# Kernel optimization log

Hardware: AMD Instinct MI355X
Metric: run time of the kernel (lower is better)

Reference implementation:

```python
import jax, jax.numpy as jnp
import numpy as np

NUM_EDGE_TYPES = 8
HIDDEN = 128
N_NODES = 50000
N_EDGES = 600000


def setup_inputs() -> dict:
    key = jax.random.key(0)
    ks = jax.random.split(key, 10)
    H = HIDDEN
    h = jax.random.normal(ks[0], (N_NODES, H), dtype=jnp.float32)
    edge_index = jax.random.randint(ks[1], (2, N_EDGES), 0, N_NODES, dtype=jnp.int32)
    edge_type = jax.random.randint(ks[2], (N_EDGES,), 0, NUM_EDGE_TYPES + 1, dtype=jnp.int32)
    s = 1.0 / np.sqrt(H)
    W_msg = jax.random.uniform(ks[3], (H, H), jnp.float32, -s, s)
    b_msg = jax.random.uniform(ks[4], (H,), jnp.float32, -s, s)
    edge_embed = jax.random.normal(ks[5], (NUM_EDGE_TYPES + 1, H), dtype=jnp.float32)
    W_ih = jax.random.uniform(ks[6], (3 * H, H), jnp.float32, -s, s)
    W_hh = jax.random.uniform(ks[7], (3 * H, H), jnp.float32, -s, s)
    b_ih = jax.random.uniform(ks[8], (3 * H,), jnp.float32, -s, s)
    b_hh = jax.random.uniform(ks[9], (3 * H,), jnp.float32, -s, s)
    return {"h": h, "edge_index": edge_index, "edge_type": edge_type,
            "num_nodes": N_NODES, "W_msg": W_msg, "b_msg": b_msg,
            "edge_embed": edge_embed, "W_ih": W_ih, "W_hh": W_hh,
            "b_ih": b_ih, "b_hh": b_hh}


def _gru_cell(x, h, W_ih, W_hh, b_ih, b_hh):
    # PyTorch GRUCell: gates ordered (r, z, n)
    H = h.shape[-1]
    gi = x @ W_ih.T + b_ih  # (N, 3H)
    gh = h @ W_hh.T + b_hh
    i_r, i_z, i_n = gi[:, :H], gi[:, H:2 * H], gi[:, 2 * H:]
    h_r, h_z, h_n = gh[:, :H], gh[:, H:2 * H], gh[:, 2 * H:]
    r = jax.nn.sigmoid(i_r + h_r)
    z = jax.nn.sigmoid(i_z + h_z)
    n = jnp.tanh(i_n + r * h_n)
    return (1.0 - z) * n + z * h


def reference(h, edge_index, edge_type, num_nodes, W_msg, b_msg, edge_embed, W_ih, W_hh, b_ih, b_hh):
    src = edge_index[0]
    dst = edge_index[1]
    # gather -> linear -> edge-type embed add
    src_h = h[src] @ W_msg.T + b_msg                      # (E, H)
    emb = edge_embed[jnp.clip(edge_type, 0, NUM_EDGE_TYPES)]  # (E, H)
    msg = src_h + emb
    # scatter-add into per-node message buffer
    messages = jax.ops.segment_sum(msg, dst, num_segments=num_nodes)  # (num_nodes, H)
    h_new = _gru_cell(messages, h[:num_nodes], W_ih, W_hh, b_ih, b_hh)
    result = jnp.zeros_like(h).at[:num_nodes].set(h_new)
    return result
```

## Files before the change

kernel.cpp:

```cpp
#include <hip/hip_runtime.h>
#include <math.h>

#define H 128
typedef unsigned int u32;
typedef unsigned long long u64;
typedef __attribute__((ext_vector_type(8))) short short8;
typedef __attribute__((ext_vector_type(4))) float floatx4;

#define XS_STRIDE 136

#define SCAN_B 64
#define SCAN_T 256

__device__ __forceinline__ float sigmoid_f(float x) {
    return 1.0f / (1.0f + __expf(-x));
}
__device__ __forceinline__ float tanh_f(float x) {
    float t = __expf(-2.0f * fabsf(x));
    float r = (1.0f - t) / (1.0f + t);
    return copysignf(r, x);
}
__device__ __forceinline__ unsigned short f2bf(float x) {
    u32 u = __float_as_uint(x);
    return (unsigned short)((u + 0x7fffu + ((u >> 16) & 1u)) >> 16);
}
__device__ __forceinline__ float bf2f(unsigned short s) {
    return __uint_as_float(((u32)s) << 16);
}
__device__ __forceinline__ float bf_lo32(u32 u) { return __uint_as_float(u << 16); }
__device__ __forceinline__ float bf_hi32(u32 u) { return __uint_as_float(u & 0xffff0000u); }

__global__ __launch_bounds__(256) void h_convert_kernel(
    const float* __restrict__ h, unsigned short* __restrict__ h_b, int total8)
{
    int idx = blockIdx.x * 256 + threadIdx.x;
    if (idx >= total8) return;
    const float4* p = (const float4*)(h + (size_t)idx * 8);
    float4 a = p[0], b = p[1];
    short8 v;
    v[0] = (short)f2bf(a.x); v[1] = (short)f2bf(a.y);
    v[2] = (short)f2bf(a.z); v[3] = (short)f2bf(a.w);
    v[4] = (short)f2bf(b.x); v[5] = (short)f2bf(b.y);
    v[6] = (short)f2bf(b.z); v[7] = (short)f2bf(b.w);
    *(short8*)(h_b + (size_t)idx * 8) = v;
}

__global__ __launch_bounds__(256) void prep_kernel(
    const float* __restrict__ Wih, const float* __restrict__ Whh,
    const float* __restrict__ Wm,  const float* __restrict__ emb,
    const float* __restrict__ bm,
    unsigned short* __restrict__ Wcs, unsigned short* __restrict__ Whhs,
    unsigned short* __restrict__ embWs)
{
    int idx = blockIdx.x * 256 + threadIdx.x;
    if (idx < 49152) {
        int g = idx >> 7;
        int k = idx & 127;
        float acc = 0.f;
#pragma unroll 4
        for (int c = 0; c < H; ++c)
            acc += Wih[(size_t)g * H + c] * Wm[(size_t)c * H + k];
        int gate = g >> 7;
        int wi = g & 127;
        int j = wi >> 4, m = wi & 15;
        int kc = k >> 5, q = (k >> 3) & 3, i = k & 7;
        int l = q * 16 + m;
        Wcs[(size_t)(((gate * 8 + j) * 4 + kc) * 64 + l) * 8 + i] = f2bf(acc);
    } else if (idx < 61440) {
        int s = idx - 49152;
        int i = s & 7;
        int l = (s >> 3) & 63;
        int jb = s >> 9;
        int gate = jb >> 3, jj = jb & 7;
        int q = l >> 4, m = l & 15;
        int t = q * 8 + i;
        unsigned short v = 0;
        if (t < 9) {
            int g = gate * 128 + jj * 16 + m;
            float acc = 0.f;
#pragma unroll 4
            for (int jx = 0; jx < H; ++jx)
                acc += (emb[(size_t)t * H + jx] + bm[jx]) * Wih[(size_t)g * H + jx];
            v = f2bf(acc);
        }
        embWs[s] = v;
    } else if (idx < 67584) {
        int t2 = idx - 61440;
        int l  = t2 & 63;
        int kc = (t2 >> 6) & 3;
        int jr = t2 >> 8;
        int m = l & 15, q = l >> 4;
        size_t srco = (size_t)(jr * 16 + m) * H + kc * 32 + q * 8;
        const float4* s0 = (const float4*)(Whh + srco);
        float4 a = s0[0], b = s0[1];
        short8 v;
        v[0] = (short)f2bf(a.x); v[1] = (short)f2bf(a.y);
        v[2] = (short)f2bf(a.z); v[3] = (short)f2bf(a.w);
        v[4] = (short)f2bf(b.x); v[5] = (short)f2bf(b.y);
        v[6] = (short)f2bf(b.z); v[7] = (short)f2bf(b.w);
        *(short8*)(Whhs + (size_t)t2 * 8) = v;
    }
}

__global__ __launch_bounds__(256) void hist_kernel(
    const int* __restrict__ eidx, int* __restrict__ deg, int E)
{
    int e = blockIdx.x * 256 + threadIdx.x;
    if (e < E) atomicAdd(&deg[eidx[E + e]], 1);
}

__global__ __launch_bounds__(SCAN_T) void scan_part_kernel(
    const int* __restrict__ deg, int* __restrict__ tsum,
    int* __restrict__ bsum, int N, int ipt)
{
    __shared__ int red[SCAN_T];
    int t = threadIdx.x;
    int g = blockIdx.x * SCAN_T + t;
    int s = g * ipt;
    int e = s + ipt < N ? s + ipt : N;
    int sum = 0;
    for (int i = s; i < e; ++i) sum += deg[i];
    tsum[g] = sum;
    red[t] = sum;
    __syncthreads();
    for (int d = SCAN_T / 2; d > 0; d >>= 1) {
        if (t < d) red[t] += red[t + d];
        __syncthreads();
    }
    if (t == 0) bsum[blockIdx.x] = red[0];
}

__global__ __launch_bounds__(SCAN_T) void scan_final_kernel(
    const int* __restrict__ deg, const int* __restrict__ tsum,
    const int* __restrict__ bsum, int* __restrict__ off,
    int* __restrict__ pos, int N, int ipt)
{
    __shared__ int part[SCAN_T];
    __shared__ int bpre[SCAN_B + 1];
    int t = threadIdx.x;
    if (t == 0) {
        int acc = 0;
        for (int b2 = 0; b2 < SCAN_B; ++b2) { bpre[b2] = acc; acc += bsum[b2]; }
        bpre[SCAN_B] = acc;
        if (blockIdx.x == 0) off[N] = acc;
    }
    int g = blockIdx.x * SCAN_T + t;
    part[t] = tsum[g];
    __syncthreads();
    for (int d = 1; d < SCAN_T; d <<= 1) {
        int v = (t >= d) ? part[t - d] : 0;
        __syncthreads();
        part[t] += v;
        __syncthreads();
    }
    int base = bpre[blockIdx.x] + ((t == 0) ? 0 : part[t - 1]);
    int s = g * ipt;
    int e = s + ipt < N ? s + ipt : N;
    for (int i = s; i < e; ++i) {
        off[i] = base;
        pos[i] = base;
        base += deg[i];
    }
}

__global__ __launch_bounds__(256) void fill_kernel(
    const int* __restrict__ eidx, const int* __restrict__ etype,
    int* __restrict__ pos, int* __restrict__ packed, int E)
{
    int e = blockIdx.x * 256 + threadIdx.x;
    if (e >= E) return;
    int src = eidx[e];
    int dst = eidx[E + e];
    int t = etype[e];
    t = t < 0 ? 0 : (t > 8 ? 8 : t);
    int p = atomicAdd(&pos[dst], 1);
    packed[p] = src | (t << 24);
}

__global__ __launch_bounds__(256) void gather_kernel(
    const unsigned short* __restrict__ h_b,
    const int* __restrict__ off, const int* __restrict__ packed,
    unsigned short* __restrict__ S_b, u64* __restrict__ cnt, int N)
{
    int n = blockIdx.x * 4 + (threadIdx.x >> 6);
    if (n >= N) return;
    int lane = threadIdx.x & 63;
    int b = off[n], e = off[n + 1];
    float ax = 0.f, ay = 0.f;
    u64 c = 0;
    int i = b;
    for (; i + 4 <= e; i += 4) {
        int u0 = packed[i + 0];
        int u1 = packed[i + 1];
        int u2 = packed[i + 2];
        int u3 = packed[i + 3];
        u32 x0 = *((const u32*)(h_b + (size_t)(u0 & 0xffffff) * H) + lane);
        u32 x1 = *((const u32*)(h_b + (size_t)(u1 & 0xffffff) * H) + lane);
        u32 x2 = *((const u32*)(h_b + (size_t)(u2 & 0xffffff) * H) + lane);
        u32 x3 = *((const u32*)(h_b + (size_t)(u3 & 0xffffff) * H) + lane);
        c += (1ull << (7 * (u0 >> 24))) + (1ull << (7 * (u1 >> 24)))
           + (1ull << (7 * (u2 >> 24))) + (1ull << (7 * (u3 >> 24)));
        ax += bf_lo32(x0) + bf_lo32(x1) + bf_lo32(x2) + bf_lo32(x3);
        ay += bf_hi32(x0) + bf_hi32(x1) + bf_hi32(x2) + bf_hi32(x3);
    }
    for (; i < e; ++i) {
        int u = packed[i];
        u32 x = *((const u32*)(h_b + (size_t)(u & 0xffffff) * H) + lane);
        c += 1ull << (7 * (u >> 24));
        ax += bf_lo32(x);
        ay += bf_hi32(x);
    }
    u32 o = (u32)f2bf(ax) | ((u32)f2bf(ay) << 16);
    *((u32*)(S_b + (size_t)n * H) + lane) = o;
    if (lane == 0) cnt[n] = c;
}

__global__ __launch_bounds__(256, 4) void gru_mfma_kernel(
    const unsigned short* __restrict__ S_b, const unsigned short* __restrict__ h_b,
    const unsigned short* __restrict__ Wcs, const unsigned short* __restrict__ Whhs,
    const unsigned short* __restrict__ embWs,
    const float* __restrict__ bih, const float* __restrict__ bhh,
    const u64* __restrict__ cnt,
    const int* __restrict__ numn, float* __restrict__ out, int N)
{
    __shared__ unsigned short xs[32 * XS_STRIDE];
    __shared__ unsigned short hsb[32 * XS_STRIDE];
    __shared__ unsigned short cs[32 * 32];

    int tid = threadIdx.x;
    int node0 = blockIdx.x * 32;

    for (int c = tid; c < 512; c += 256) {
        int r = c >> 4;
        int k8 = (c & 15) << 3;
        int n = node0 + r;
        int nc = n < N ? n : N - 1;
        *(short8*)(&xs[r * XS_STRIDE + k8]) =
            *(const short8*)(S_b + (size_t)nc * H + k8);
        *(short8*)(&hsb[r * XS_STRIDE + k8]) =
            *(const short8*)(h_b + (size_t)nc * H + k8);
    }
    for (int c2 = tid; c2 < 1024; c2 += 256) {
        int r = c2 >> 5, t = c2 & 31;
        int n = node0 + r;
        u64 cv = cnt[n < N ? n : N - 1];
        cs[c2] = (t < 9) ? f2bf((float)((u32)(cv >> (7 * t)) & 127u))
                         : (unsigned short)0;
    }
    __syncthreads();

    int lane = tid & 63;
    int wv = tid >> 6;
    int rg = wv & 1;
    int jhalf = wv >> 1;
    int am = lane & 15;
    int aq = lane >> 4;

    short8 ax[4], ahf[4];
    int arow = rg * 16 + am;
#pragma unroll
    for (int kc = 0; kc < 4; ++kc) {
        ax[kc]  = *(const short8*)(&xs[arow * XS_STRIDE + kc * 32 + aq * 8]);
        ahf[kc] = *(const short8*)(&hsb[arow * XS_STRIDE + kc * 32 + aq * 8]);
    }
    short8 acn = *(const short8*)(&cs[arow * 32 + aq * 8]);

    int num_nodes = numn[0];
    floatx4 zero = {0.f, 0.f, 0.f, 0.f};

#pragma unroll
    for (int jt = 0; jt < 4; ++jt) {
        int j = jhalf * 4 + jt;
        floatx4 aIr = zero, aHr = zero, aIz = zero, aHz = zero, aIn = zero, aHn = zero;
        {
            short8 er = *(const short8*)(embWs + (size_t)((0 * 8 + j) * 64 + lane) * 8);
            short8 ez = *(const short8*)(embWs + (size_t)((1 * 8 + j) * 64 + lane) * 8);
            short8 en = *(const short8*)(embWs + (size_t)((2 * 8 + j) * 64 + lane) * 8);
            aIr = __builtin_amdgcn_mfma_f32_16x16x32_bf16(acn, er, aIr, 0, 0, 0);
            aIz = __builtin_amdgcn_mfma_f32_16x16x32_bf16(acn, ez, aIz, 0, 0, 0);
            aIn = __builtin_amdgcn_mfma_f32_16x16x32_bf16(acn, en, aIn, 0, 0, 0);
        }
#pragma unroll
        for (int kc = 0; kc < 4; ++kc) {
            size_t c_r = (size_t)(((0 * 8 + j) * 4 + kc) * 64 + lane) * 8;
            size_t c_z = (size_t)(((1 * 8 + j) * 4 + kc) * 64 + lane) * 8;
            size_t c_n = (size_t)(((2 * 8 + j) * 4 + kc) * 64 + lane) * 8;
            short8 bir = *(const short8*)(Wcs + c_r);
            short8 bhr = *(const short8*)(Whhs + c_r);
            short8 biz = *(const short8*)(Wcs + c_z);
            short8 bhz = *(const short8*)(Whhs + c_z);
            short8 bin = *(const short8*)(Wcs + c_n);
            short8 bhn = *(const short8*)(Whhs + c_n);
            aIr = __builtin_amdgcn_mfma_f32_16x16x32_bf16(ax[kc],  bir, aIr, 0, 0, 0);
            aHr = __builtin_amdgcn_mfma_f32_16x16x32_bf16(ahf[kc], bhr, aHr, 0, 0, 0);
            aIz = __builtin_amdgcn_mfma_f32_16x16x32_bf16(ax[kc],  biz, aIz, 0, 0, 0);
            aHz = __builtin_amdgcn_mfma_f32_16x16x32_bf16(ahf[kc], bhz, aHz, 0, 0, 0);
            aIn = __builtin_amdgcn_mfma_f32_16x16x32_bf16(ax[kc],  bin, aIn, 0, 0, 0);
            aHn = __builtin_amdgcn_mfma_f32_16x16x32_bf16(ahf[kc], bhn, aHn, 0, 0, 0);
        }
        int c = j * 16 + am;
        float b_ir = bih[c],       b_hr = bhh[c];
        float b_iz = bih[128 + c], b_hz = bhh[128 + c];
        float b_in = bih[256 + c], b_hn = bhh[256 + c];
#pragma unroll
        for (int q = 0; q < 4; ++q) {
            int m = aq * 4 + q;
            int node = node0 + rg * 16 + m;
            if (node < N) {
                float r  = sigmoid_f(aIr[q] + b_ir + aHr[q] + b_hr);
                float z  = sigmoid_f(aIz[q] + b_iz + aHz[q] + b_hz);
                float nv = tanh_f((aIn[q] + b_in) + r * (aHn[q] + b_hn));
                float hv = bf2f(hsb[(rg * 16 + m) * XS_STRIDE + c]);
                float o  = (1.0f - z) * nv + z * hv;
                out[(size_t)node * H + c] = (node < num_nodes) ? o : 0.0f;
            }
        }
    }
}

extern "C" void kernel_launch(void* const* d_in, const int* in_sizes, int n_in,
                              void* d_out, int out_size, void* d_ws, size_t ws_size,
                              hipStream_t stream) {
    const float* h    = (const float*)d_in[0];
    const int*  eidx  = (const int*)d_in[1];
    const int*  etype = (const int*)d_in[2];
    const int*  numn  = (const int*)d_in[3];
    const float* Wm   = (const float*)d_in[4];
    const float* bm   = (const float*)d_in[5];
    const float* emb  = (const float*)d_in[6];
    const float* Wih  = (const float*)d_in[7];
    const float* Whh  = (const float*)d_in[8];
    const float* bih  = (const float*)d_in[9];
    const float* bhh  = (const float*)d_in[10];

    int N = in_sizes[0] / H;
    int E = in_sizes[2];

    unsigned short* S_b   = (unsigned short*)d_ws;
    unsigned short* h_b   = S_b + (size_t)N * H;
    unsigned short* Wcs   = h_b + (size_t)N * H;
    unsigned short* Whhs  = Wcs + 3 * H * H;
    unsigned short* embWs = Whhs + 3 * H * H;
    u64* cnt    = (u64*)(embWs + 12288);
    int* deg    = (int*)(cnt + N);
    int* pos    = deg + N;
    int* off    = pos + N;
    int* packed = off + (N + 1);
    int* tsum   = packed + E;
    int* bsum   = tsum + SCAN_B * SCAN_T;

    hipMemsetAsync(deg, 0, (size_t)N * sizeof(int), stream);

    int total8 = N * H / 8;
    h_convert_kernel<<<(total8 + 255) / 256, 256, 0, stream>>>(h, h_b, total8);
    prep_kernel<<<264, 256, 0, stream>>>(Wih, Whh, Wm, emb, bm, Wcs, Whhs, embWs);
    hist_kernel<<<(E + 255) / 256, 256, 0, stream>>>(eidx, deg, E);

    int ipt = (N + SCAN_B * SCAN_T - 1) / (SCAN_B * SCAN_T);
    scan_part_kernel<<<SCAN_B, SCAN_T, 0, stream>>>(deg, tsum, bsum, N, ipt);
    scan_final_kernel<<<SCAN_B, SCAN_T, 0, stream>>>(deg, tsum, bsum, off, pos, N, ipt);

    fill_kernel<<<(E + 255) / 256, 256, 0, stream>>>(eidx, etype, pos, packed, E);

    gather_kernel<<<(N + 3) / 4, 256, 0, stream>>>(h_b, off, packed, S_b, cnt, N);

    int nblk32 = (N + 31) / 32;
    gru_mfma_kernel<<<nblk32, 256, 0, stream>>>(S_b, h_b, Wcs, Whhs, embWs,
                                                bih, bhh, cnt, numn, (float*)d_out, N);
}
```

Before: 237.8 us.

## Fuse preprocessing kernels and retile GRU kernel to 64 nodes per block

Merges the h-to-bf16 conversion, the degree-buffer zeroing (replacing hipMemsetAsync) and the weight prep into one launch, which removes launch and memset overhead. The GRU MFMA kernel now processes 64 nodes per block, with each wave owning two output column tiles across all four row tiles. Each loaded weight fragment is therefore reused across four MFMA row tiles, cutting global weight traffic per node. The cost is more accumulator registers (72 floats per lane for the six gates times four tiles), which may hurt occupancy under launch_bounds(256,4), and A fragments are now re-read from LDS inside the loop.

```diff
diff --git a/kernel.cpp b/kernel.cpp
--- a/kernel.cpp
+++ b/kernel.cpp
@@ -8,6 +8,7 @@
 typedef __attribute__((ext_vector_type(4))) float floatx4;
 
 #define XS_STRIDE 136
+#define CS_STRIDE 40
 
 #define SCAN_B 64
 #define SCAN_T 256
@@ -30,29 +31,35 @@
 __device__ __forceinline__ float bf_lo32(u32 u) { return __uint_as_float(u << 16); }
 __device__ __forceinline__ float bf_hi32(u32 u) { return __uint_as_float(u & 0xffff0000u); }
 
-__global__ __launch_bounds__(256) void h_convert_kernel(
-    const float* __restrict__ h, unsigned short* __restrict__ h_b, int total8)
-{
-    int idx = blockIdx.x * 256 + threadIdx.x;
-    if (idx >= total8) return;
-    const float4* p = (const float4*)(h + (size_t)idx * 8);
-    float4 a = p[0], b = p[1];
-    short8 v;
-    v[0] = (short)f2bf(a.x); v[1] = (short)f2bf(a.y);
-    v[2] = (short)f2bf(a.z); v[3] = (short)f2bf(a.w);
-    v[4] = (short)f2bf(b.x); v[5] = (short)f2bf(b.y);
-    v[6] = (short)f2bf(b.z); v[7] = (short)f2bf(b.w);
-    *(short8*)(h_b + (size_t)idx * 8) = v;
-}
-
-__global__ __launch_bounds__(256) void prep_kernel(
+__global__ __launch_bounds__(256) void fused_pre_kernel(
+    const float* __restrict__ h, unsigned short* __restrict__ h_b, int total8,
+    int* __restrict__ deg, int N,
     const float* __restrict__ Wih, const float* __restrict__ Whh,
     const float* __restrict__ Wm,  const float* __restrict__ emb,
     const float* __restrict__ bm,
     unsigned short* __restrict__ Wcs, unsigned short* __restrict__ Whhs,
-    unsigned short* __restrict__ embWs)
-{
-    int idx = blockIdx.x * 256 + threadIdx.x;
+    unsigned short* __restrict__ embWs, int HB, int DB)
+{
+    int b = blockIdx.x;
+    if (b < HB) {
+        int idx = b * 256 + threadIdx.x;
+        if (idx >= total8) return;
+        const float4* p = (const float4*)(h + (size_t)idx * 8);
+        float4 a = p[0], bb = p[1];
+        short8 v;
+        v[0] = (short)f2bf(a.x);  v[1] = (short)f2bf(a.y);
+        v[2] = (short)f2bf(a.z);  v[3] = (short)f2bf(a.w);
+        v[4] = (short)f2bf(bb.x); v[5] = (short)f2bf(bb.y);
+        v[6] = (short)f2bf(bb.z); v[7] = (short)f2bf(bb.w);
+        *(short8*)(h_b + (size_t)idx * 8) = v;
+        return;
+    }
+    if (b < HB + DB) {
+        int idx = (b - HB) * 256 + threadIdx.x;
+        if (idx < N) deg[idx] = 0;
+        return;
+    }
+    int idx = (b - HB - DB) * 256 + threadIdx.x;
     if (idx < 49152) {
         int g = idx >> 7;
         int k = idx & 127;
@@ -92,12 +99,12 @@
         int m = l & 15, q = l >> 4;
         size_t srco = (size_t)(jr * 16 + m) * H + kc * 32 + q * 8;
         const float4* s0 = (const float4*)(Whh + srco);
-        float4 a = s0[0], b = s0[1];
+        float4 a = s0[0], bb = s0[1];
         short8 v;
-        v[0] = (short)f2bf(a.x); v[1] = (short)f2bf(a.y);
-        v[2] = (short)f2bf(a.z); v[3] = (short)f2bf(a.w);
-        v[4] = (short)f2bf(b.x); v[5] = (short)f2bf(b.y);
-        v[6] = (short)f2bf(b.z); v[7] = (short)f2bf(b.w);
+        v[0] = (short)f2bf(a.x);  v[1] = (short)f2bf(a.y);
+        v[2] = (short)f2bf(a.z);  v[3] = (short)f2bf(a.w);
+        v[4] = (short)f2bf(bb.x); v[5] = (short)f2bf(bb.y);
+        v[6] = (short)f2bf(bb.z); v[7] = (short)f2bf(bb.w);
         *(short8*)(Whhs + (size_t)t2 * 8) = v;
     }
 }
@@ -223,14 +230,14 @@
     const u64* __restrict__ cnt,
     const int* __restrict__ numn, float* __restrict__ out, int N)
 {
-    __shared__ unsigned short xs[32 * XS_STRIDE];
-    __shared__ unsigned short hsb[32 * XS_STRIDE];
-    __shared__ unsigned short cs[32 * 32];
+    __shared__ unsigned short xs[64 * XS_STRIDE];
+    __shared__ unsigned short hsb[64 * XS_STRIDE];
+    __shared__ unsigned short cs[64 * CS_STRIDE];
 
     int tid = threadIdx.x;
-    int node0 = blockIdx.x * 32;
-
-    for (int c = tid; c < 512; c += 256) {
+    int node0 = blockIdx.x * 64;
+
+    for (int c = tid; c < 1024; c += 256) {
         int r = c >> 4;
         int k8 = (c & 15) << 3;
         int n = node0 + r;
@@ -240,45 +247,46 @@
         *(short8*)(&hsb[r * XS_STRIDE + k8]) =
             *(const short8*)(h_b + (size_t)nc * H + k8);
     }
-    for (int c2 = tid; c2 < 1024; c2 += 256) {
-        int r = c2 >> 5, t = c2 & 31;
+    {
+        int r = tid >> 2, tg = tid & 3;
         int n = node0 + r;
         u64 cv = cnt[n < N ? n : N - 1];
-        cs[c2] = (t < 9) ? f2bf((float)((u32)(cv >> (7 * t)) & 127u))
-                         : (unsigned short)0;
+        short8 v = {0, 0, 0, 0, 0, 0, 0, 0};
+        if (tg == 0) {
+#pragma unroll
+            for (int i = 0; i < 8; ++i)
+                v[i] = (short)f2bf((float)((u32)(cv >> (7 * i)) & 127u));
+        } else if (tg == 1) {
+            v[0] = (short)f2bf((float)((u32)(cv >> 56) & 127u));
+        }
+        *(short8*)(&cs[r * CS_STRIDE + tg * 8]) = v;
     }
     __syncthreads();
 
     int lane = tid & 63;
     int wv = tid >> 6;
-    int rg = wv & 1;
-    int jhalf = wv >> 1;
     int am = lane & 15;
     int aq = lane >> 4;
 
-    short8 ax[4], ahf[4];
-    int arow = rg * 16 + am;
-#pragma unroll
-    for (int kc = 0; kc < 4; ++kc) {
-        ax[kc]  = *(const short8*)(&xs[arow * XS_STRIDE + kc * 32 + aq * 8]);
-        ahf[kc] = *(const short8*)(&hsb[arow * XS_STRIDE + kc * 32 + aq * 8]);
-    }
-    short8 acn = *(const short8*)(&cs[arow * 32 + aq * 8]);
-
     int num_nodes = numn[0];
     floatx4 zero = {0.f, 0.f, 0.f, 0.f};
 
 #pragma unroll
-    for (int jt = 0; jt < 4; ++jt) {
-        int j = jhalf * 4 + jt;
-        floatx4 aIr = zero, aHr = zero, aIz = zero, aHz = zero, aIn = zero, aHn = zero;
+    for (int jj = 0; jj < 2; ++jj) {
+        int j = wv * 2 + jj;
+        floatx4 aIr[4], aHr[4], aIz[4], aHz[4], aIn[4], aHn[4];
         {
             short8 er = *(const short8*)(embWs + (size_t)((0 * 8 + j) * 64 + lane) * 8);
             short8 ez = *(const short8*)(embWs + (size_t)((1 * 8 + j) * 64 + lane) * 8);
             short8 en = *(const short8*)(embWs + (size_t)((2 * 8 + j) * 64 + lane) * 8);
-            aIr = __builtin_amdgcn_mfma_f32_16x16x32_bf16(acn, er, aIr, 0, 0, 0);
-            aIz = __builtin_amdgcn_mfma_f32_16x16x32_bf16(acn, ez, aIz, 0, 0, 0);
-            aIn = __builtin_amdgcn_mfma_f32_16x16x32_bf16(acn, en, aIn, 0, 0, 0);
+#pragma unroll
+            for (int rt = 0; rt < 4; ++rt) {
+                short8 acn = *(const short8*)(&cs[(rt * 16 + am) * CS_STRIDE + aq * 8]);
+                aIr[rt] = __builtin_amdgcn_mfma_f32_16x16x32_bf16(acn, er, zero, 0, 0, 0);
+                aIz[rt] = __builtin_amdgcn_mfma_f32_16x16x32_bf16(acn, ez, zero, 0, 0, 0);
+                aIn[rt] = __builtin_amdgcn_mfma_f32_16x16x32_bf16(acn, en, zero, 0, 0, 0);
+                aHr[rt] = zero; aHz[rt] = zero; aHn[rt] = zero;
+            }
         }
 #pragma unroll
         for (int kc = 0; kc < 4; ++kc) {
@@ -291,28 +299,37 @@
             short8 bhz = *(const short8*)(Whhs + c_z);
             short8 bin = *(const short8*)(Wcs + c_n);
             short8 bhn = *(const short8*)(Whhs + c_n);
-            aIr = __builtin_amdgcn_mfma_f32_16x16x32_bf16(ax[kc],  bir, aIr, 0, 0, 0);
-            aHr = __builtin_amdgcn_mfma_f32_16x16x32_bf16(ahf[kc], bhr, aHr, 0, 0, 0);
-            aIz = __builtin_amdgcn_mfma_f32_16x16x32_bf16(ax[kc],  biz, aIz, 0, 0, 0);
-            aHz = __builtin_amdgcn_mfma_f32_16x16x32_bf16(ahf[kc], bhz, aHz, 0, 0, 0);
-            aIn = __builtin_amdgcn_mfma_f32_16x16x32_bf16(ax[kc],  bin, aIn, 0, 0, 0);
-            aHn = __builtin_amdgcn_mfma_f32_16x16x32_bf16(ahf[kc], bhn, aHn, 0, 0, 0);
+#pragma unroll
+            for (int rt = 0; rt < 4; ++rt) {
+                int arow = rt * 16 + am;
+                short8 axv = *(const short8*)(&xs[arow * XS_STRIDE + kc * 32 + aq * 8]);
+                short8 ahv = *(const short8*)(&hsb[arow * XS_STRIDE + kc * 32 + aq * 8]);
+                aIr[rt] = __builtin_amdgcn_mfma_f32_16x16x32_bf16(axv, bir, aIr[rt], 0, 0, 0);
+                aHr[rt] = __builtin_amdgcn_mfma_f32_16x16x32_bf16(ahv, bhr, aHr[rt], 0, 0, 0);
+                aIz[rt] = __builtin_amdgcn_mfma_f32_16x16x32_bf16(axv, biz, aIz[rt], 0, 0, 0);
+                aHz[rt] = __builtin_amdgcn_mfma_f32_16x16x32_bf16(ahv, bhz, aHz[rt], 0, 0, 0);
+                aIn[rt] = __builtin_amdgcn_mfma_f32_16x16x32_bf16(axv, bin, aIn[rt], 0, 0, 0);
+                aHn[rt] = __builtin_amdgcn_mfma_f32_16x16x32_bf16(ahv, bhn, aHn[rt], 0, 0, 0);
+            }
         }
         int c = j * 16 + am;
         float b_ir = bih[c],       b_hr = bhh[c];
         float b_iz = bih[128 + c], b_hz = bhh[128 + c];
         float b_in = bih[256 + c], b_hn = bhh[256 + c];
 #pragma unroll
-        for (int q = 0; q < 4; ++q) {
-            int m = aq * 4 + q;
-            int node = node0 + rg * 16 + m;
-            if (node < N) {
-                float r  = sigmoid_f(aIr[q] + b_ir + aHr[q] + b_hr);
-                float z  = sigmoid_f(aIz[q] + b_iz + aHz[q] + b_hz);
-                float nv = tanh_f((aIn[q] + b_in) + r * (aHn[q] + b_hn));
-                float hv = bf2f(hsb[(rg * 16 + m) * XS_STRIDE + c]);
-                float o  = (1.0f - z) * nv + z * hv;
-                out[(size_t)node * H + c] = (node < num_nodes) ? o : 0.0f;
+        for (int rt = 0; rt < 4; ++rt) {
+#pragma unroll
+            for (int q = 0; q < 4; ++q) {
+                int m = rt * 16 + aq * 4 + q;
+                int node = node0 + m;
+                if (node < N) {
+                    float r  = sigmoid_f(aIr[rt][q] + b_ir + aHr[rt][q] + b_hr);
+                    float z  = sigmoid_f(aIz[rt][q] + b_iz + aHz[rt][q] + b_hz);
+                    float nv = tanh_f((aIn[rt][q] + b_in) + r * (aHn[rt][q] + b_hn));
+                    float hv = bf2f(hsb[m * XS_STRIDE + c]);
+                    float o  = (1.0f - z) * nv + z * hv;
+                    out[(size_t)node * H + c] = (node < num_nodes) ? o : 0.0f;
+                }
             }
         }
     }
@@ -349,11 +366,13 @@
     int* tsum   = packed + E;
     int* bsum   = tsum + SCAN_B * SCAN_T;
 
-    hipMemsetAsync(deg, 0, (size_t)N * sizeof(int), stream);
-
     int total8 = N * H / 8;
-    h_convert_kernel<<<(total8 + 255) / 256, 256, 0, stream>>>(h, h_b, total8);
-    prep_kernel<<<264, 256, 0, stream>>>(Wih, Whh, Wm, emb, bm, Wcs, Whhs, embWs);
+    int HB = (total8 + 255) / 256;
+    int DB = (N + 255) / 256;
+    int PB = 264;
+    fused_pre_kernel<<<HB + DB + PB, 256, 0, stream>>>(
+        h, h_b, total8, deg, N, Wih, Whh, Wm, emb, bm, Wcs, Whhs, embWs, HB, DB);
+
     hist_kernel<<<(E + 255) / 256, 256, 0, stream>>>(eidx, deg, E);
 
     int ipt = (N + SCAN_B * SCAN_T - 1) / (SCAN_B * SCAN_T);
@@ -364,7 +383,7 @@
 
     gather_kernel<<<(N + 3) / 4, 256, 0, stream>>>(h_b, off, packed, S_b, cnt, N);
 
-    int nblk32 = (N + 31) / 32;
-    gru_mfma_kernel<<<nblk32, 256, 0, stream>>>(S_b, h_b, Wcs, Whhs, embWs,
+    int nblk64 = (N + 63) / 64;
+    gru_mfma_kernel<<<nblk64, 256, 0, stream>>>(S_b, h_b, Wcs, Whhs, embWs,
                                                 bih, bhh, cnt, numn, (float*)d_out, N);
 }
```

Measured after the change: 280.3 us. +17.9%, slower.
